# Performance work log

Hardware: AMD Instinct MI355X
Metric: run time of the kernel (lower is better)

The kernel has to match this reference:

```python
import jax, jax.numpy as jnp
import numpy as np

# 0-indexed channel groups (fixed constants from the source)
_G1 = np.array([2, 1, 3, 4, 5, 7, 8, 9, 10, 11, 12, 13]) - 1
_G2 = np.array([6, 14, 15, 16, 22, 23, 24, 25, 31, 32, 33, 34, 40, 41, 42, 43, 49, 50]) - 1
_G3 = np.array([17, 18, 19, 20, 21, 26, 27, 28, 29, 30, 35, 36, 37, 38, 39, 44, 45, 46, 47, 48]) - 1
_G4 = np.array([51, 52, 53, 54, 55, 56, 57, 58, 59, 60, 61, 62]) - 1
_GROUPS = [_G1, _G2, _G3, _G4]

B, DIM, NCLS = 2048, 512, 62
_CHN = [12, 18, 20, 12]


def setup_inputs() -> dict:
    key = jax.random.key(0)
    ks = jax.random.split(key, 20)
    inp = {}
    for i, ch in enumerate(_CHN):
        inp[f"x_{i+1}"] = jax.random.normal(ks[i], (B, ch, DIM), dtype=jnp.float32)
    inp["g"] = jax.random.normal(ks[4], (B, NCLS, DIM), dtype=jnp.float32)
    for i in range(4):
        inp[f"logits_{i+1}"] = jax.random.normal(ks[5 + i], (B, NCLS), dtype=jnp.float32)
    for i, ch in enumerate(_CHN):
        fan_in = DIM * ch
        bound = 1.0 / np.sqrt(fan_in)
        inp[f"W{i+1}"] = jax.random.uniform(ks[9 + 2 * i], (fan_in, 1), minval=-bound, maxval=bound, dtype=jnp.float32)
        inp[f"b{i+1}"] = jax.random.uniform(ks[10 + 2 * i], (1,), minval=-bound, maxval=bound, dtype=jnp.float32)
    return inp


def _confidence(logits):
    # confidence = max_prob * (1 - normalized_entropy), shape [B, 1]
    p = jax.nn.softmax(logits, axis=1)
    max_p = p.max(axis=1)
    ent = -jnp.sum(p * jnp.log(p + 1e-8), axis=1)
    norm_ent = ent / jnp.log(jnp.float32(logits.shape[1]))
    return (max_p * (1.0 - norm_ent))[:, None]


def reference(x_1, x_2, x_3, x_4, g, logits_1, logits_2, logits_3, logits_4,
              W1, b1, W2, b2, W3, b3, W4, b4):
    Bsz = x_1.shape[0]
    confs = jnp.concatenate([_confidence(l) for l in (logits_1, logits_2, logits_3, logits_4)], axis=1)  # [B,4]
    norm_conf = jax.nn.softmax(confs, axis=1)
    xs = (x_1, x_2, x_3, x_4)
    Ws = (W1, W2, W3, W4)
    bs = (b1, b2, b3, b4)
    trans = jnp.zeros_like(g)
    for i in range(4):
        u = jax.nn.sigmoid(xs[i].reshape(Bsz, -1) @ Ws[i] + bs[i])  # [B,1]
        u_final = u * norm_conf[:, i:i + 1]                          # [B,1]
        x_region = g[:, _GROUPS[i], :]                               # gather [B,ch,dim]
        x_total = (xs[i] + x_region) * u_final[:, :, None]
        trans = trans.at[:, _GROUPS[i], :].set(x_total)              # scatter (index_copy)
    return (norm_conf[:, 0:1], norm_conf[:, 1:2], norm_conf[:, 2:3], norm_conf[:, 3:4], trans)
```

## Files before the change

### kernel.cpp

```cpp
#include <hip/hip_runtime.h>
#include <math.h>

#define BATCH 2048
#define NCLS 62
#define TPB 512

__device__ __forceinline__ float wave_max(float v) {
#pragma unroll
    for (int m = 32; m >= 1; m >>= 1) v = fmaxf(v, __shfl_xor(v, m, 64));
    return v;
}
__device__ __forceinline__ float wave_sum(float v) {
#pragma unroll
    for (int m = 32; m >= 1; m >>= 1) v += __shfl_xor(v, m, 64);
    return v;
}

__device__ const unsigned char GRP_TBL[62] = {
    0,0,0,0,0, 1, 0,0,0,0,0,0,0,
    1,1,1,
    2,2,2,2,2,
    1,1,1,1,
    2,2,2,2,2,
    1,1,1,1,
    2,2,2,2,2,
    1,1,1,1,
    2,2,2,2,2,
    1,1,
    3,3,3,3,3,3,3,3,3,3,3,3
};
__device__ const unsigned char CHAN_TBL[62] = {
    1,0,2,3,4, 0, 5,6,7,8,9,10,11,
    1,2,3,
    0,1,2,3,4,
    4,5,6,7,
    5,6,7,8,9,
    8,9,10,11,
    10,11,12,13,14,
    12,13,14,15,
    15,16,17,18,19,
    16,17,
    0,1,2,3,4,5,6,7,8,9,10,11
};

__global__ __launch_bounds__(TPB) void fused_kernel(
    const float4* __restrict__ x1, const float4* __restrict__ x2,
    const float4* __restrict__ x3, const float4* __restrict__ x4,
    const float4* __restrict__ g,
    const float* __restrict__ lg1, const float* __restrict__ lg2,
    const float* __restrict__ lg3, const float* __restrict__ lg4,
    const float4* __restrict__ W1, const float* __restrict__ bb1,
    const float4* __restrict__ W2, const float* __restrict__ bb2,
    const float4* __restrict__ W3, const float* __restrict__ bb3,
    const float4* __restrict__ W4, const float* __restrict__ bb4,
    float* __restrict__ out_nc, float4* __restrict__ out_trans)
{
    __shared__ float4 x_s[7936];
    __shared__ float conf_s[4];
    __shared__ float part_s[8][4];
    __shared__ float s_s[4];

    const int b    = blockIdx.x;
    const int tid  = threadIdx.x;
    const int wave = tid >> 6;
    const int lane = tid & 63;

    const int fan4[4]  = {1536, 2304, 2560, 1536};
    const int base4[4] = {0, 1536, 3840, 6400};
    const float4* xv[4] = {x1, x2, x3, x4};
    const float4* wv[4] = {W1, W2, W3, W4};

    float acc0 = 0.f, acc1 = 0.f, acc2 = 0.f, acc3 = 0.f;
#pragma unroll
    for (int i = 0; i < 4; ++i) {
        const float4* xp = xv[i] + (size_t)b * fan4[i];
        const float4* wp = wv[i];
        float a = 0.f;
#pragma unroll 4
        for (int j = tid; j < fan4[i]; j += TPB) {
            float4 xx = xp[j];
            float4 ww = wp[j];
            x_s[base4[i] + j] = xx;
            a += xx.x * ww.x + xx.y * ww.y + xx.z * ww.z + xx.w * ww.w;
        }
        if (i == 0) acc0 = a; else if (i == 1) acc1 = a;
        else if (i == 2) acc2 = a; else acc3 = a;
    }
    {
        float a0 = wave_sum(acc0);
        float a1 = wave_sum(acc1);
        float a2 = wave_sum(acc2);
        float a3 = wave_sum(acc3);
        if (lane == 0) {
            part_s[wave][0] = a0; part_s[wave][1] = a1;
            part_s[wave][2] = a2; part_s[wave][3] = a3;
        }
    }

    if (wave < 4) {
        const float* lg = (wave == 0) ? lg1 : (wave == 1) ? lg2
                        : (wave == 2) ? lg3 : lg4;
        float v = (lane < NCLS) ? lg[b * NCLS + lane] : -INFINITY;
        float m = wave_max(v);
        float e = (lane < NCLS) ? __expf(v - m) : 0.0f;
        float S = wave_sum(e);
        float p = e / S;
        float t = (lane < NCLS) ? p * __logf(p + 1e-8f) : 0.0f;
        float ent = -wave_sum(t);
        float conf = (1.0f / S) * (1.0f - ent * 0.242298797f);
        if (lane == 0) conf_s[wave] = conf;
    }
    __syncthreads();

    if (tid < 4) {
        const int i = tid;
        float dot = 0.f;
#pragma unroll
        for (int w = 0; w < 8; ++w) dot += part_s[w][i];
        float bias = (i == 0) ? bb1[0] : (i == 1) ? bb2[0]
                   : (i == 2) ? bb3[0] : bb4[0];
        float u = 1.0f / (1.0f + __expf(-(dot + bias)));
        float c0 = conf_s[0], c1 = conf_s[1], c2 = conf_s[2], c3 = conf_s[3];
        float m4 = fmaxf(fmaxf(c0, c1), fmaxf(c2, c3));
        float e0 = __expf(c0 - m4), e1 = __expf(c1 - m4);
        float e2 = __expf(c2 - m4), e3 = __expf(c3 - m4);
        float S4 = e0 + e1 + e2 + e3;
        float ei = (i == 0) ? e0 : (i == 1) ? e1 : (i == 2) ? e2 : e3;
        float nc = ei / S4;
        out_nc[i * BATCH + b] = nc;
        s_s[i] = u * nc;
    }
    __syncthreads();

    const float4* gp = g + (size_t)b * 7936;
    float4*       op = out_trans + (size_t)b * 7936;
#pragma unroll 4
    for (int k = 0; k < 16; ++k) {
        int idx = tid + k * TPB;
        if (idx < 7936) {
            int row = idx >> 7;
            int d4  = idx & 127;
            int grp = GRP_TBL[row];
            int ch  = CHAN_TBL[row];
            float sc = s_s[grp];
            float4 xx = x_s[base4[grp] + ch * 128 + d4];
            float4 gg = gp[idx];
            float4 o;
            o.x = (xx.x + gg.x) * sc;
            o.y = (xx.y + gg.y) * sc;
            o.z = (xx.z + gg.z) * sc;
            o.w = (xx.w + gg.w) * sc;
            op[idx] = o;
        }
    }
}

extern "C" void kernel_launch(void* const* d_in, const int* in_sizes, int n_in,
                              void* d_out, int out_size, void* d_ws, size_t ws_size,
                              hipStream_t stream) {
    const float* x1  = (const float*)d_in[0];
    const float* x2  = (const float*)d_in[1];
    const float* x3  = (const float*)d_in[2];
    const float* x4  = (const float*)d_in[3];
    const float* g   = (const float*)d_in[4];
    const float* lg1 = (const float*)d_in[5];
    const float* lg2 = (const float*)d_in[6];
    const float* lg3 = (const float*)d_in[7];
    const float* lg4 = (const float*)d_in[8];
    const float* W1  = (const float*)d_in[9];
    const float* b1  = (const float*)d_in[10];
    const float* W2  = (const float*)d_in[11];
    const float* b2  = (const float*)d_in[12];
    const float* W3  = (const float*)d_in[13];
    const float* b3  = (const float*)d_in[14];
    const float* W4  = (const float*)d_in[15];
    const float* b4  = (const float*)d_in[16];

    float* out = (float*)d_out;
    float4* out_trans = (float4*)(out + 4 * BATCH);

    fused_kernel<<<BATCH, TPB, 0, stream>>>(
        (const float4*)x1, (const float4*)x2, (const float4*)x3, (const float4*)x4,
        (const float4*)g,
        lg1, lg2, lg3, lg4,
        (const float4*)W1, b1, (const float4*)W2, b2,
        (const float4*)W3, b3, (const float4*)W4, b4,
        out, out_trans);
}
```

Baseline: 648.4 us.

## Split each batch row into four per-group blocks with register-held inputs

Launches one 256-thread block per (batch, channel group) pair instead of one 512-thread block per batch row. Each block keeps its group's x values in registers instead of a 124 KB shared-memory staging buffer, which allows higher occupancy and more blocks in flight. Each group block computes only its own dot product and writes the output rows of its group directly. The cost is that the logits confidence softmax is recomputed four times per row and the per-group blocks do unequal amounts of work.

```diff
diff --git a/kernel.cpp b/kernel.cpp
--- a/kernel.cpp
+++ b/kernel.cpp
@@ -3,7 +3,7 @@
 
 #define BATCH 2048
 #define NCLS 62
-#define TPB 512
+#define TPB 256
 
 __device__ __forceinline__ float wave_max(float v) {
 #pragma unroll
@@ -16,31 +16,11 @@
     return v;
 }
 
-__device__ const unsigned char GRP_TBL[62] = {
-    0,0,0,0,0, 1, 0,0,0,0,0,0,0,
-    1,1,1,
-    2,2,2,2,2,
-    1,1,1,1,
-    2,2,2,2,2,
-    1,1,1,1,
-    2,2,2,2,2,
-    1,1,1,1,
-    2,2,2,2,2,
-    1,1,
-    3,3,3,3,3,3,3,3,3,3,3,3
-};
-__device__ const unsigned char CHAN_TBL[62] = {
-    1,0,2,3,4, 0, 5,6,7,8,9,10,11,
-    1,2,3,
-    0,1,2,3,4,
-    4,5,6,7,
-    5,6,7,8,9,
-    8,9,10,11,
-    10,11,12,13,14,
-    12,13,14,15,
-    15,16,17,18,19,
-    16,17,
-    0,1,2,3,4,5,6,7,8,9,10,11
+__device__ const unsigned char ROWS_TBL[4][20] = {
+    { 1, 0, 2, 3, 4, 6, 7, 8, 9,10,11,12,  0,0,0,0,0,0,0,0},
+    { 5,13,14,15,21,22,23,24,30,31,32,33, 39,40,41,42,48,49, 0,0},
+    {16,17,18,19,20,25,26,27,28,29,34,35, 36,37,38,43,44,45,46,47},
+    {50,51,52,53,54,55,56,57,58,59,60,61,  0,0,0,0,0,0,0,0}
 };
 
 __global__ __launch_bounds__(TPB) void fused_kernel(
@@ -55,49 +35,41 @@
     const float4* __restrict__ W4, const float* __restrict__ bb4,
     float* __restrict__ out_nc, float4* __restrict__ out_trans)
 {
-    __shared__ float4 x_s[7936];
-    __shared__ float conf_s[4];
-    __shared__ float part_s[8][4];
-    __shared__ float s_s[4];
-
-    const int b    = blockIdx.x;
+    const int bid  = blockIdx.x;
+    const int b    = bid >> 2;
+    const int grp  = bid & 3;
     const int tid  = threadIdx.x;
     const int wave = tid >> 6;
     const int lane = tid & 63;
 
-    const int fan4[4]  = {1536, 2304, 2560, 1536};
-    const int base4[4] = {0, 1536, 3840, 6400};
-    const float4* xv[4] = {x1, x2, x3, x4};
-    const float4* wv[4] = {W1, W2, W3, W4};
+    __shared__ float conf_s[4];
+    __shared__ float part_s[4];
+    __shared__ float s_sh;
 
-    float acc0 = 0.f, acc1 = 0.f, acc2 = 0.f, acc3 = 0.f;
+    const int fan4_tbl[4] = {1536, 2304, 2560, 1536};
+    const int nj_tbl[4]   = {6, 9, 10, 6};
+    const float4* xs = (grp == 0) ? x1 : (grp == 1) ? x2 : (grp == 2) ? x3 : x4;
+    const float4* ws = (grp == 0) ? W1 : (grp == 1) ? W2 : (grp == 2) ? W3 : W4;
+    const int fan4 = fan4_tbl[grp];
+    const int nj   = nj_tbl[grp];
+
+    float4 xr[10];
+    const float4* xp = xs + (size_t)b * fan4;
+    float a = 0.f;
 #pragma unroll
-    for (int i = 0; i < 4; ++i) {
-        const float4* xp = xv[i] + (size_t)b * fan4[i];
-        const float4* wp = wv[i];
-        float a = 0.f;
-#pragma unroll 4
-        for (int j = tid; j < fan4[i]; j += TPB) {
+    for (int k = 0; k < 10; ++k) {
+        if (k < nj) {
+            int j = tid + k * TPB;
             float4 xx = xp[j];
-            float4 ww = wp[j];
-            x_s[base4[i] + j] = xx;
+            float4 ww = ws[j];
+            xr[k] = xx;
             a += xx.x * ww.x + xx.y * ww.y + xx.z * ww.z + xx.w * ww.w;
         }
-        if (i == 0) acc0 = a; else if (i == 1) acc1 = a;
-        else if (i == 2) acc2 = a; else acc3 = a;
     }
+    a = wave_sum(a);
+    if (lane == 0) part_s[wave] = a;
+
     {
-        float a0 = wave_sum(acc0);
-        float a1 = wave_sum(acc1);
-        float a2 = wave_sum(acc2);
-        float a3 = wave_sum(acc3);
-        if (lane == 0) {
-            part_s[wave][0] = a0; part_s[wave][1] = a1;
-            part_s[wave][2] = a2; part_s[wave][3] = a3;
-        }
-    }
-
-    if (wave < 4) {
         const float* lg = (wave == 0) ? lg1 : (wave == 1) ? lg2
                         : (wave == 2) ? lg3 : lg4;
         float v = (lane < NCLS) ? lg[b * NCLS + lane] : -INFINITY;
@@ -112,45 +84,46 @@
     }
     __syncthreads();
 
-    if (tid < 4) {
-        const int i = tid;
-        float dot = 0.f;
-#pragma unroll
-        for (int w = 0; w < 8; ++w) dot += part_s[w][i];
-        float bias = (i == 0) ? bb1[0] : (i == 1) ? bb2[0]
-                   : (i == 2) ? bb3[0] : bb4[0];
+    if (tid == 0) {
+        float dot = part_s[0] + part_s[1] + part_s[2] + part_s[3];
+        float bias = (grp == 0) ? bb1[0] : (grp == 1) ? bb2[0]
+                   : (grp == 2) ? bb3[0] : bb4[0];
         float u = 1.0f / (1.0f + __expf(-(dot + bias)));
         float c0 = conf_s[0], c1 = conf_s[1], c2 = conf_s[2], c3 = conf_s[3];
         float m4 = fmaxf(fmaxf(c0, c1), fmaxf(c2, c3));
         float e0 = __expf(c0 - m4), e1 = __expf(c1 - m4);
         float e2 = __expf(c2 - m4), e3 = __expf(c3 - m4);
         float S4 = e0 + e1 + e2 + e3;
-        float ei = (i == 0) ? e0 : (i == 1) ? e1 : (i == 2) ? e2 : e3;
-        float nc = ei / S4;
-        out_nc[i * BATCH + b] = nc;
-        s_s[i] = u * nc;
+        float eg = (grp == 0) ? e0 : (grp == 1) ? e1 : (grp == 2) ? e2 : e3;
+        s_sh = u * (eg / S4);
+        if (grp == 0) {
+            out_nc[0 * BATCH + b] = e0 / S4;
+            out_nc[1 * BATCH + b] = e1 / S4;
+            out_nc[2 * BATCH + b] = e2 / S4;
+            out_nc[3 * BATCH + b] = e3 / S4;
+        }
     }
     __syncthreads();
+    const float sc = s_sh;
 
     const float4* gp = g + (size_t)b * 7936;
     float4*       op = out_trans + (size_t)b * 7936;
-#pragma unroll 4
-    for (int k = 0; k < 16; ++k) {
-        int idx = tid + k * TPB;
-        if (idx < 7936) {
-            int row = idx >> 7;
-            int d4  = idx & 127;
-            int grp = GRP_TBL[row];
-            int ch  = CHAN_TBL[row];
-            float sc = s_s[grp];
-            float4 xx = x_s[base4[grp] + ch * 128 + d4];
-            float4 gg = gp[idx];
-            float4 o;
-            o.x = (xx.x + gg.x) * sc;
-            o.y = (xx.y + gg.y) * sc;
-            o.z = (xx.z + gg.z) * sc;
-            o.w = (xx.w + gg.w) * sc;
-            op[idx] = o;
+#pragma unroll
+    for (int k = 0; k < 10; ++k) {
+        if (k < nj) {
+            int j   = tid + k * TPB;
+            int ch  = j >> 7;
+            int d4  = j & 127;
+            int row = ROWS_TBL[grp][ch];
+            int o   = row * 128 + d4;
+            float4 gg = gp[o];
+            float4 xx = xr[k];
+            float4 oo;
+            oo.x = (xx.x + gg.x) * sc;
+            oo.y = (xx.y + gg.y) * sc;
+            oo.z = (xx.z + gg.z) * sc;
+            oo.w = (xx.w + gg.w) * sc;
+            op[o] = oo;
         }
     }
 }
@@ -179,7 +152,7 @@
     float* out = (float*)d_out;
     float4* out_trans = (float4*)(out + 4 * BATCH);
 
-    fused_kernel<<<BATCH, TPB, 0, stream>>>(
+    fused_kernel<<<BATCH * 4, TPB, 0, stream>>>(
         (const float4*)x1, (const float4*)x2, (const float4*)x3, (const float4*)x4,
         (const float4*)g,
         lg1, lg2, lg3, lg4,
```

Measured after the change: 619.4 us. 4.5% less time.
